# Kernel tuning notes

Hardware: AMD Instinct MI355X
Metric: run time of the kernel (lower is better)

Reference implementation:

```python
import jax, jax.numpy as jnp
import numpy as np

B = 16384      # batch
IN = 151       # input dim (layer_widths[0])
HID = 200      # RBF out_features (layer_widths[1])
CENT = 2000    # layer_centres[0]


def setup_inputs() -> dict:
    key = jax.random.key(0)
    ks = jax.random.split(key, 6)
    x = jax.random.normal(ks[0], (B, IN), dtype=jnp.float32)
    # RBF params per reset_parameters: centres ~ N(0, 0.01), sigmas = 2
    centres = 0.01 * jax.random.normal(ks[1], (HID, IN), dtype=jnp.float32)
    sigmas = jnp.full((HID,), 2.0, dtype=jnp.float32)
    # Linear layers (torch layout: weight is (out, in))
    w1 = jax.random.normal(ks[2], (CENT, HID), dtype=jnp.float32) / jnp.sqrt(jnp.float32(HID))
    b1 = jnp.zeros((CENT,), dtype=jnp.float32)
    # small scale so exp() stays well-conditioned
    w2 = 0.001 * jax.random.normal(ks[3], (CENT, CENT), dtype=jnp.float32)
    b2 = jnp.zeros((CENT,), dtype=jnp.float32)
    # kernel matrix (151, 2000); positive so Ehat[:, 0] > 0
    kern = jax.random.uniform(ks[4], (IN, CENT), dtype=jnp.float32)
    return {"x": x, "centres": centres, "sigmas": sigmas,
            "w1": w1, "b1": b1, "w2": w2, "b2": b2, "kern": kern}


def reference(x, centres, sigmas, w1, b1, w2, b2, kern):
    # RBF layer: distances_ij = ||x_i - c_j||_2 * sigma_j ; phi = exp(-distances^2)
    # exp(-(sqrt(d2)*sigma)^2) == exp(-d2 * sigma^2), so we skip the sqrt and the
    # (B, CENT, IN) expand tensor entirely.
    x2 = jnp.sum(x * x, axis=1, keepdims=True)            # (B, 1)
    c2 = jnp.sum(centres * centres, axis=1)[None, :]      # (1, HID)
    d2 = jnp.maximum(x2 + c2 - 2.0 * (x @ centres.T), 0.0)  # (B, HID)
    phi = jnp.exp(-d2 * (sigmas * sigmas)[None, :])       # (B, HID)

    h = jax.nn.relu(phi @ w1.T + b1)                      # (B, CENT)
    out = jnp.exp(h @ w2.T + b2)                          # (B, CENT)

    Ehat = out @ kern.T                                   # (B, IN)  == matmul(kern, out.T).T
    Rhat = out / Ehat[:, :1]                              # divide by correction term Ehat[:, 0]
    Ehat2 = Rhat @ kern.T                                 # (B, IN)
    return (Ehat2, Rhat, Ehat2, Rhat, x)
```

## Files before the change

### kernel.cpp

```cpp
#include <hip/hip_runtime.h>

#define BDIM 16384
#define IN_D 151
#define HID_D 200
#define CENT_D 2000

#define INP 192
#define HIDP 256
#define CENTP 2048
#define KERNR 256

using bf16x8 = __attribute__((ext_vector_type(8))) short;
using f32x4  = __attribute__((ext_vector_type(4))) float;
using f4     = __attribute__((ext_vector_type(4))) float;
using us4    = __attribute__((ext_vector_type(4))) unsigned short;
using us8    = __attribute__((ext_vector_type(8))) unsigned short;
using i32x4  = __attribute__((ext_vector_type(4))) int;
using i32x8  = __attribute__((ext_vector_type(8))) int;

__device__ __forceinline__ unsigned short f2bf(float f) {
  unsigned u = __builtin_bit_cast(unsigned, f);
  u += 0x7FFFu + ((u >> 16) & 1u);
  return (unsigned short)(u >> 16);
}
__device__ __forceinline__ float bf2f(unsigned short h) {
  unsigned u = ((unsigned)h) << 16;
  return __builtin_bit_cast(float, u);
}
__device__ __forceinline__ unsigned char f2fp8(float f) {
  return (unsigned char)(__builtin_amdgcn_cvt_pk_fp8_f32(f, f, 0, false) & 0xFF);
}

typedef __attribute__((address_space(1))) const unsigned int guint;
typedef __attribute__((address_space(3))) unsigned int luint;
__device__ __forceinline__ void g2l16(const void* g, void* l) {
  __builtin_amdgcn_global_load_lds((guint*)g, (luint*)l, 16, 0, 0);
}

struct GArgs {
  const unsigned short* A;
  const unsigned short* B;
  int K;
  int kspan;
  const float* x2; const float* c2; const float* sg2;
  const float* bias;
  unsigned short* obf; int ldo;
  unsigned char* o8;
  float* of;
};

template<int MODE>
__global__ __launch_bounds__(256) void gemm_bt(GArgs p) {
  __shared__ __align__(16) short As[128 * 64];
  __shared__ __align__(16) short Bs[128 * 64];
  const int tid  = threadIdx.x;
  const int lane = tid & 63;
  const int w    = tid >> 6;
  const int wr   = w >> 1, wc = w & 1;
  const int lr   = lane & 15;
  const int tm = blockIdx.x, tn = blockIdx.y;
  const int K = p.K;
  const int kbeg = blockIdx.z * p.kspan;
  f32x4 acc[4][4] = {};

  const unsigned short* Ag = p.A + (size_t)tm * 128 * K;
  const unsigned short* Bg = p.B + (size_t)tn * 128 * K;

  int rowc[4], colc[4], ldsc[4];
#pragma unroll
  for (int i = 0; i < 4; i++) {
    int cc = i * 256 + tid;
    rowc[i] = cc >> 3;
    colc[i] = ((cc & 7) ^ (rowc[i] & 7)) * 8;
    ldsc[i] = cc * 8;
  }

  for (int k0 = kbeg; k0 < kbeg + p.kspan; k0 += 64) {
    __syncthreads();
#pragma unroll
    for (int i = 0; i < 4; i++)
      g2l16(Ag + (size_t)rowc[i] * K + k0 + colc[i], &As[ldsc[i]]);
#pragma unroll
    for (int i = 0; i < 4; i++)
      g2l16(Bg + (size_t)rowc[i] * K + k0 + colc[i], &Bs[ldsc[i]]);
    __syncthreads();
#pragma unroll
    for (int ks = 0; ks < 2; ks++) {
      bf16x8 af[4], bfr[4];
#pragma unroll
      for (int m = 0; m < 4; m++) {
        int r = wr * 64 + m * 16 + lr;
        af[m] = *(const bf16x8*)&As[r * 64 + ((((ks << 2) + (lane >> 4)) ^ (r & 7)) << 3)];
      }
#pragma unroll
      for (int n = 0; n < 4; n++) {
        int r = wc * 64 + n * 16 + lr;
        bfr[n] = *(const bf16x8*)&Bs[r * 64 + ((((ks << 2) + (lane >> 4)) ^ (r & 7)) << 3)];
      }
#pragma unroll
      for (int m = 0; m < 4; m++)
#pragma unroll
        for (int n = 0; n < 4; n++)
          acc[m][n] = __builtin_amdgcn_mfma_f32_16x16x32_bf16(af[m], bfr[n], acc[m][n], 0, 0, 0);
    }
  }

  const int rb = tm * 128 + wr * 64 + (lane >> 4) * 4;
  const int cb = tn * 128 + wc * 64 + lr;
#pragma unroll
  for (int m = 0; m < 4; m++) {
#pragma unroll
    for (int n = 0; n < 4; n++) {
#pragma unroll
      for (int r = 0; r < 4; r++) {
        const int gi = rb + m * 16 + r;
        const int gj = cb + n * 16;
        const float v = acc[m][n][r];
        if constexpr (MODE == 0) {
          float ph = 0.f;
          if (gj < HID_D) {
            float d2 = fmaxf(p.x2[gi] + p.c2[gj] - 2.f * v, 0.f);
            ph = __expf(-d2 * p.sg2[gj]);
          }
          p.obf[(size_t)gi * p.ldo + gj] = f2bf(ph);
        } else if constexpr (MODE == 1) {
          float b = (gj < CENT_D) ? p.bias[gj] : 0.f;
          p.o8[(size_t)gi * p.ldo + gj] = f2fp8(fmaxf(v + b, 0.f));
        } else {
          float* of = p.of + (size_t)blockIdx.z * BDIM * IN_D;
          if (gj < IN_D) of[(size_t)gi * IN_D + gj] = v;
        }
      }
    }
  }
}

struct G8Args {
  const unsigned char* A;
  const unsigned char* B;
  int K;
  const float* bias;
  unsigned short* obf; int ldo;
};

__global__ __launch_bounds__(256) void gemm_fp8(G8Args p) {
  __shared__ __align__(16) unsigned char As[128 * 128];
  __shared__ __align__(16) unsigned char Bs[128 * 128];
  const int tid  = threadIdx.x;
  const int lane = tid & 63;
  const int w    = tid >> 6;
  const int wr   = w >> 1, wc = w & 1;
  const int lr   = lane & 15;
  const int g    = lane >> 4;
  const int tm = blockIdx.x, tn = blockIdx.y;
  const int K = p.K;
  f32x4 acc[4][4] = {};

  const unsigned char* Ag = p.A + (size_t)tm * 128 * K;
  const unsigned char* Bg = p.B + (size_t)tn * 128 * K;

  int rowc[4], colb[4], ldsb[4];
#pragma unroll
  for (int i = 0; i < 4; i++) {
    int cc = i * 256 + tid;
    rowc[i] = cc >> 3;
    colb[i] = ((cc & 7) ^ (rowc[i] & 7)) << 4;
    ldsb[i] = cc << 4;
  }

  for (int k0 = 0; k0 < K; k0 += 128) {
    __syncthreads();
#pragma unroll
    for (int i = 0; i < 4; i++)
      g2l16(Ag + (size_t)rowc[i] * K + k0 + colb[i], &As[ldsb[i]]);
#pragma unroll
    for (int i = 0; i < 4; i++)
      g2l16(Bg + (size_t)rowc[i] * K + k0 + colb[i], &Bs[ldsb[i]]);
    __syncthreads();

    i32x8 bfr[4];
#pragma unroll
    for (int n = 0; n < 4; n++) {
      const int r = wc * 64 + n * 16 + lr;
      const int rb_ = r << 7, rx = r & 7;
      i32x4 lo = *(const i32x4*)&Bs[rb_ + (((2 * g) ^ rx) << 4)];
      i32x4 hi = *(const i32x4*)&Bs[rb_ + (((2 * g + 1) ^ rx) << 4)];
      bfr[n][0] = lo[0]; bfr[n][1] = lo[1]; bfr[n][2] = lo[2]; bfr[n][3] = lo[3];
      bfr[n][4] = hi[0]; bfr[n][5] = hi[1]; bfr[n][6] = hi[2]; bfr[n][7] = hi[3];
    }
#pragma unroll
    for (int m = 0; m < 4; m++) {
      const int r = wr * 64 + m * 16 + lr;
      const int rb_ = r << 7, rx = r & 7;
      i32x4 lo = *(const i32x4*)&As[rb_ + (((2 * g) ^ rx) << 4)];
      i32x4 hi = *(const i32x4*)&As[rb_ + (((2 * g + 1) ^ rx) << 4)];
      i32x8 av;
      av[0] = lo[0]; av[1] = lo[1]; av[2] = lo[2]; av[3] = lo[3];
      av[4] = hi[0]; av[5] = hi[1]; av[6] = hi[2]; av[7] = hi[3];
#pragma unroll
      for (int n = 0; n < 4; n++)
        acc[m][n] = __builtin_amdgcn_mfma_scale_f32_16x16x128_f8f6f4(
            av, bfr[n], acc[m][n], 0, 0, 0, 127, 0, 127);
    }
  }

  const int rb = tm * 128 + wr * 64 + (lane >> 4) * 4;
  const int cb = tn * 128 + wc * 64 + lr;
  const float rs = 1.0f / 256.0f;
#pragma unroll
  for (int m = 0; m < 4; m++) {
#pragma unroll
    for (int n = 0; n < 4; n++) {
      const int gj = cb + n * 16;
#pragma unroll
      for (int r = 0; r < 4; r++) {
        const int gi = rb + m * 16 + r;
        float o = (gj < CENT_D) ? __expf(acc[m][n][r] * rs + p.bias[gj]) : 0.f;
        p.obf[(size_t)gi * p.ldo + gj] = f2bf(o);
      }
    }
  }
}

__global__ __launch_bounds__(256) void prep_cast(
    const float* __restrict__ x, const float* __restrict__ cen,
    const float* __restrict__ w1, const float* __restrict__ kern,
    unsigned short* __restrict__ x_bf, unsigned short* __restrict__ c_bf,
    unsigned short* __restrict__ w1p, unsigned short* __restrict__ kernp) {
  const int c = blockIdx.x * 256 + threadIdx.x;
  const float* src; unsigned short* dst; int R, C, cpq, local, vec;
  if (c < 786432)       { src = x;    dst = x_bf;  R = 16384; C = 151;  cpq = 48;  local = c;           vec = 0; }
  else if (c < 798720)  { src = cen;  dst = c_bf;  R = 200;   C = 151;  cpq = 48;  local = c - 786432;  vec = 0; }
  else if (c < 929792)  { src = w1;   dst = w1p;   R = 2000;  C = 200;  cpq = 64;  local = c - 798720;  vec = 1; }
  else                  { src = kern; dst = kernp; R = 151;   C = 2000; cpq = 512; local = c - 929792;  vec = 1; }
  const int r  = local / cpq;
  const int c4 = (local - r * cpq) << 2;
  us4 o;
  if (vec && r < R && c4 + 3 < C) {
    f4 v = *(const f4*)&src[(size_t)r * C + c4];
    o[0] = f2bf(v[0]); o[1] = f2bf(v[1]); o[2] = f2bf(v[2]); o[3] = f2bf(v[3]);
  } else {
#pragma unroll
    for (int k = 0; k < 4; k++) {
      float v = (r < R && c4 + k < C) ? src[(size_t)r * C + c4 + k] : 0.f;
      o[k] = f2bf(v);
    }
  }
  *(us4*)&dst[(size_t)local * 4] = o;
}

__global__ __launch_bounds__(256) void cast_fp8(
    const float* __restrict__ src, unsigned char* __restrict__ dst) {
  const int i = blockIdx.x * 256 + threadIdx.x;
  const int r = i >> 9;
  const int c4 = (i & 511) << 2;
  float v0 = 0.f, v1 = 0.f, v2 = 0.f, v3 = 0.f;
  if (r < 2000 && c4 + 3 < 2000) {
    f4 v = *(const f4*)&src[(size_t)r * 2000 + c4];
    v0 = v[0] * 256.f; v1 = v[1] * 256.f; v2 = v[2] * 256.f; v3 = v[3] * 256.f;
  } else if (r < 2000) {
    if (c4 + 0 < 2000) v0 = src[(size_t)r * 2000 + c4 + 0] * 256.f;
    if (c4 + 1 < 2000) v1 = src[(size_t)r * 2000 + c4 + 1] * 256.f;
    if (c4 + 2 < 2000) v2 = src[(size_t)r * 2000 + c4 + 2] * 256.f;
    if (c4 + 3 < 2000) v3 = src[(size_t)r * 2000 + c4 + 3] * 256.f;
  }
  int p0 = __builtin_amdgcn_cvt_pk_fp8_f32(v0, v1, 0, false);
  int p1 = __builtin_amdgcn_cvt_pk_fp8_f32(v2, v3, 0, false);
  unsigned int packed = ((unsigned)p0 & 0xFFFFu) | (((unsigned)p1 & 0xFFFFu) << 16);
  *(unsigned int*)&dst[(size_t)i * 4] = packed;
}

__global__ __launch_bounds__(256) void prep_misc(
    const float* __restrict__ x, const float* __restrict__ cen,
    const float* __restrict__ sg,
    float* __restrict__ x2, float* __restrict__ c2, float* __restrict__ sg2) {
  const int b = blockIdx.x;
  if (b == 4160) {
    int j = threadIdx.x;
    sg2[j] = (j < HID_D) ? sg[j] * sg[j] : 0.f;
    return;
  }
  const float* src; float* dst; int R, base;
  if (b < 4096) { src = x;   dst = x2; R = BDIM;  base = b * 4; }
  else          { src = cen; dst = c2; R = HID_D; base = (b - 4096) * 4; }
  const int row = base + (threadIdx.x >> 6);
  const int l = threadIdx.x & 63;
  float s = 0.f;
  if (row < R)
    for (int k = l; k < IN_D; k += 64) { float v = src[(size_t)row * IN_D + k]; s += v * v; }
#pragma unroll
  for (int off = 32; off > 0; off >>= 1) s += __shfl_down(s, off);
  if (l == 0) dst[row] = s;
}

__global__ __launch_bounds__(256) void finalize(
    float* __restrict__ dout, const unsigned short* __restrict__ outp,
    const float* __restrict__ x, const float* __restrict__ part) {
  const int i = blockIdx.x;
  const size_t SL = (size_t)BDIM * IN_D;
  float* Eh = dout;
  float* Ra = dout + SL;
  float* Eb = dout + SL + (size_t)BDIM * CENT_D;
  float* Rb = Eb + SL;
  float* xo = Rb + (size_t)BDIM * CENT_D;
  const size_t ib = (size_t)i * IN_D;
  const float e0 = part[ib] + part[SL + ib] + part[2 * SL + ib] + part[3 * SL + ib];
  const float s = 1.f / e0;
  const int t = threadIdx.x;
  if (t < IN_D) {
    float v = (part[ib + t] + part[SL + ib + t] + part[2 * SL + ib + t] + part[3 * SL + ib + t]) * s;
    Eh[ib + t] = v;
    Eb[ib + t] = v;
    xo[ib + t] = x[ib + t];
  }
  if (t < 250) {
    const us8 u = *(const us8*)&outp[(size_t)i * CENTP + t * 8];
    f4 a, b;
#pragma unroll
    for (int k = 0; k < 4; k++) a[k] = bf2f(u[k]) * s;
#pragma unroll
    for (int k = 0; k < 4; k++) b[k] = bf2f(u[4 + k]) * s;
    const size_t o = (size_t)i * CENT_D + t * 8;
    *(f4*)&Ra[o] = a; *(f4*)&Ra[o + 4] = b;
    *(f4*)&Rb[o] = a; *(f4*)&Rb[o + 4] = b;
  }
}

extern "C" void kernel_launch(void* const* d_in, const int* in_sizes, int n_in,
                              void* d_out, int out_size, void* d_ws, size_t ws_size,
                              hipStream_t stream) {
  (void)in_sizes; (void)n_in; (void)out_size; (void)ws_size;
  const float* x       = (const float*)d_in[0];
  const float* centres = (const float*)d_in[1];
  const float* sigmas  = (const float*)d_in[2];
  const float* w1      = (const float*)d_in[3];
  const float* b1      = (const float*)d_in[4];
  const float* w2      = (const float*)d_in[5];
  const float* b2      = (const float*)d_in[6];
  const float* kern    = (const float*)d_in[7];
  float* dout = (float*)d_out;

  char* ws = (char*)d_ws;
  size_t off = 0;
  auto alloc = [&](size_t bytes) {
    char* p = ws + off;
    off = (off + bytes + 255) & ~(size_t)255;
    return p;
  };
  unsigned short* x_bf  = (unsigned short*)alloc((size_t)BDIM * INP * 2);
  unsigned short* c_bf  = (unsigned short*)alloc((size_t)KERNR * INP * 2);
  unsigned short* w1p   = (unsigned short*)alloc((size_t)CENTP * HIDP * 2);
  unsigned char*  w2p8  = (unsigned char*)alloc((size_t)CENTP * CENTP);
  unsigned short* kernp = (unsigned short*)alloc((size_t)KERNR * CENTP * 2);
  unsigned short* phip  = (unsigned short*)alloc((size_t)BDIM * HIDP * 2);
  unsigned short* outp  = (unsigned short*)alloc((size_t)BDIM * CENTP * 2);
  float* x2  = (float*)alloc((size_t)BDIM * 4);
  float* c2  = (float*)alloc((size_t)KERNR * 4);
  float* sg2 = (float*)alloc((size_t)KERNR * 4);
  float* eparts = (float*)alloc((size_t)4 * BDIM * IN_D * 4);
  unsigned char* hp8 = (unsigned char*)(dout + (size_t)BDIM * (2 * IN_D + CENT_D));

  prep_cast<<<4144, 256, 0, stream>>>(x, centres, w1, kern, x_bf, c_bf, w1p, kernp);
  cast_fp8<<<4096, 256, 0, stream>>>(w2, w2p8);
  prep_misc<<<4161, 256, 0, stream>>>(x, centres, sigmas, x2, c2, sg2);

  GArgs g0{}; g0.A = x_bf; g0.B = c_bf; g0.K = INP; g0.kspan = INP;
  g0.x2 = x2; g0.c2 = c2; g0.sg2 = sg2; g0.obf = phip; g0.ldo = HIDP;
  gemm_bt<0><<<dim3(BDIM / 128, HIDP / 128, 1), 256, 0, stream>>>(g0);

  GArgs g1{}; g1.A = phip; g1.B = w1p; g1.K = HIDP; g1.kspan = HIDP;
  g1.bias = b1; g1.o8 = hp8; g1.ldo = CENTP;
  gemm_bt<1><<<dim3(BDIM / 128, CENTP / 128, 1), 256, 0, stream>>>(g1);

  G8Args g2{}; g2.A = hp8; g2.B = w2p8; g2.K = CENTP;
  g2.bias = b2; g2.obf = outp; g2.ldo = CENTP;
  gemm_fp8<<<dim3(BDIM / 128, CENTP / 128), 256, 0, stream>>>(g2);

  GArgs g3{}; g3.A = outp; g3.B = kernp; g3.K = CENTP; g3.kspan = CENTP / 4;
  g3.of = eparts;
  gemm_bt<3><<<dim3(BDIM / 128, KERNR / 128, 4), 256, 0, stream>>>(g3);

  finalize<<<BDIM, 256, 0, stream>>>(dout, outp, x, eparts);
}
```

Baseline: 280.3 us.

## Quantize hidden activations and second weight matrix to FP4 with FP8 first layer

The RBF output phi and the first-layer weights are now stored as FP8, so the first linear layer runs on the FP8 scaled MFMA. Its ReLU output h is packed to FP4 (two values per byte via a lane shuffle). The large second GEMM then runs as an FP4 x FP4 scaled MFMA against a 512-scaled FP4 copy of w2. This halves operand bytes for the dominant GEMM and uses the higher-rate FP4 matrix path. In exchange it adds heavy quantization error from a coarse 8-level FP4 grid applied to both h and w2, a branchy software FP4 encoder in the epilogue, and zero-padded halves in the MFMA operand registers.

```diff
diff --git a/kernel.cpp b/kernel.cpp
--- a/kernel.cpp
+++ b/kernel.cpp
@@ -30,6 +30,20 @@
 __device__ __forceinline__ unsigned char f2fp8(float f) {
   return (unsigned char)(__builtin_amdgcn_cvt_pk_fp8_f32(f, f, 0, false) & 0xFF);
 }
+__device__ __forceinline__ unsigned f2fp4(float f) {
+  float a = fabsf(f);
+  unsigned s = (__builtin_bit_cast(unsigned, f) >> 31) << 3;
+  unsigned m;
+  if      (a < 0.25f) m = 0;
+  else if (a < 0.75f) m = 1;
+  else if (a < 1.25f) m = 2;
+  else if (a < 1.75f) m = 3;
+  else if (a < 2.5f)  m = 4;
+  else if (a < 3.5f)  m = 5;
+  else if (a < 5.0f)  m = 6;
+  else                m = 7;
+  return s | m;
+}
 
 typedef __attribute__((address_space(1))) const unsigned int guint;
 typedef __attribute__((address_space(3))) unsigned int luint;
@@ -43,9 +57,7 @@
   int K;
   int kspan;
   const float* x2; const float* c2; const float* sg2;
-  const float* bias;
-  unsigned short* obf; int ldo;
-  unsigned char* o8;
+  unsigned char* o8; int ldo;
   float* of;
 };
 
@@ -122,10 +134,7 @@
             float d2 = fmaxf(p.x2[gi] + p.c2[gj] - 2.f * v, 0.f);
             ph = __expf(-d2 * p.sg2[gj]);
           }
-          p.obf[(size_t)gi * p.ldo + gj] = f2bf(ph);
-        } else if constexpr (MODE == 1) {
-          float b = (gj < CENT_D) ? p.bias[gj] : 0.f;
-          p.o8[(size_t)gi * p.ldo + gj] = f2fp8(fmaxf(v + b, 0.f));
+          p.o8[(size_t)gi * p.ldo + gj] = f2fp8(ph);
         } else {
           float* of = p.of + (size_t)blockIdx.z * BDIM * IN_D;
           if (gj < IN_D) of[(size_t)gi * IN_D + gj] = v;
@@ -135,15 +144,14 @@
   }
 }
 
-struct G8Args {
+struct GhArgs {
   const unsigned char* A;
   const unsigned char* B;
-  int K;
   const float* bias;
-  unsigned short* obf; int ldo;
+  unsigned char* o4;
 };
 
-__global__ __launch_bounds__(256) void gemm_fp8(G8Args p) {
+__global__ __launch_bounds__(256) void gemm_h(GhArgs p) {
   __shared__ __align__(16) unsigned char As[128 * 128];
   __shared__ __align__(16) unsigned char Bs[128 * 128];
   const int tid  = threadIdx.x;
@@ -153,11 +161,10 @@
   const int lr   = lane & 15;
   const int g    = lane >> 4;
   const int tm = blockIdx.x, tn = blockIdx.y;
-  const int K = p.K;
   f32x4 acc[4][4] = {};
 
-  const unsigned char* Ag = p.A + (size_t)tm * 128 * K;
-  const unsigned char* Bg = p.B + (size_t)tn * 128 * K;
+  const unsigned char* Ag = p.A + (size_t)tm * 128 * 256;
+  const unsigned char* Bg = p.B + (size_t)tn * 128 * 256;
 
   int rowc[4], colb[4], ldsb[4];
 #pragma unroll
@@ -168,14 +175,15 @@
     ldsb[i] = cc << 4;
   }
 
-  for (int k0 = 0; k0 < K; k0 += 128) {
-    __syncthreads();
-#pragma unroll
-    for (int i = 0; i < 4; i++)
-      g2l16(Ag + (size_t)rowc[i] * K + k0 + colb[i], &As[ldsb[i]]);
-#pragma unroll
-    for (int i = 0; i < 4; i++)
-      g2l16(Bg + (size_t)rowc[i] * K + k0 + colb[i], &Bs[ldsb[i]]);
+#pragma unroll
+  for (int k0 = 0; k0 < 256; k0 += 128) {
+    __syncthreads();
+#pragma unroll
+    for (int i = 0; i < 4; i++)
+      g2l16(Ag + (size_t)rowc[i] * 256 + k0 + colb[i], &As[ldsb[i]]);
+#pragma unroll
+    for (int i = 0; i < 4; i++)
+      g2l16(Bg + (size_t)rowc[i] * 256 + k0 + colb[i], &Bs[ldsb[i]]);
     __syncthreads();
 
     i32x8 bfr[4];
@@ -206,7 +214,98 @@
 
   const int rb = tm * 128 + wr * 64 + (lane >> 4) * 4;
   const int cb = tn * 128 + wc * 64 + lr;
-  const float rs = 1.0f / 256.0f;
+  const float rs = 0.125f;
+#pragma unroll
+  for (int m = 0; m < 4; m++) {
+#pragma unroll
+    for (int n = 0; n < 4; n++) {
+      const int gj = cb + n * 16;
+      const float b = (gj < CENT_D) ? p.bias[gj] : 0.f;
+#pragma unroll
+      for (int r = 0; r < 4; r++) {
+        const int gi = rb + m * 16 + r;
+        float hv = fmaxf(acc[m][n][r] * rs + b, 0.f);
+        float ov = __shfl_xor(hv, 1);
+        if (!(lane & 1))
+          p.o4[(size_t)gi * 1024 + (gj >> 1)] =
+              (unsigned char)(f2fp4(hv) | (f2fp4(ov) << 4));
+      }
+    }
+  }
+}
+
+struct G4Args {
+  const unsigned char* A;
+  const unsigned char* B;
+  const float* bias;
+  unsigned short* obf;
+};
+
+__global__ __launch_bounds__(256) void gemm_fp4(G4Args p) {
+  __shared__ __align__(16) unsigned char As[128 * 128];
+  __shared__ __align__(16) unsigned char Bs[128 * 128];
+  const int tid  = threadIdx.x;
+  const int lane = tid & 63;
+  const int w    = tid >> 6;
+  const int wr   = w >> 1, wc = w & 1;
+  const int lr   = lane & 15;
+  const int g    = lane >> 4;
+  const int tm = blockIdx.x, tn = blockIdx.y;
+  const int KB = CENTP / 2;
+  f32x4 acc[4][4] = {};
+
+  const unsigned char* Ag = p.A + (size_t)tm * 128 * KB;
+  const unsigned char* Bg = p.B + (size_t)tn * 128 * KB;
+
+  int rowc[4], colb[4], ldsb[4];
+#pragma unroll
+  for (int i = 0; i < 4; i++) {
+    int cc = i * 256 + tid;
+    rowc[i] = cc >> 3;
+    colb[i] = ((cc & 7) ^ (rowc[i] & 7)) << 4;
+    ldsb[i] = cc << 4;
+  }
+
+  for (int kb0 = 0; kb0 < KB; kb0 += 128) {
+    __syncthreads();
+#pragma unroll
+    for (int i = 0; i < 4; i++)
+      g2l16(Ag + (size_t)rowc[i] * KB + kb0 + colb[i], &As[ldsb[i]]);
+#pragma unroll
+    for (int i = 0; i < 4; i++)
+      g2l16(Bg + (size_t)rowc[i] * KB + kb0 + colb[i], &Bs[ldsb[i]]);
+    __syncthreads();
+
+#pragma unroll
+    for (int ks = 0; ks < 2; ks++) {
+      i32x8 bfr[4];
+#pragma unroll
+      for (int n = 0; n < 4; n++) {
+        const int r = wc * 64 + n * 16 + lr;
+        const int rb_ = r << 7, rx = r & 7;
+        i32x4 v = *(const i32x4*)&Bs[rb_ + ((((ks << 2) + g) ^ rx) << 4)];
+        bfr[n][0] = v[0]; bfr[n][1] = v[1]; bfr[n][2] = v[2]; bfr[n][3] = v[3];
+        bfr[n][4] = 0; bfr[n][5] = 0; bfr[n][6] = 0; bfr[n][7] = 0;
+      }
+#pragma unroll
+      for (int m = 0; m < 4; m++) {
+        const int r = wr * 64 + m * 16 + lr;
+        const int rb_ = r << 7, rx = r & 7;
+        i32x4 v = *(const i32x4*)&As[rb_ + ((((ks << 2) + g) ^ rx) << 4)];
+        i32x8 av;
+        av[0] = v[0]; av[1] = v[1]; av[2] = v[2]; av[3] = v[3];
+        av[4] = 0; av[5] = 0; av[6] = 0; av[7] = 0;
+#pragma unroll
+        for (int n = 0; n < 4; n++)
+          acc[m][n] = __builtin_amdgcn_mfma_scale_f32_16x16x128_f8f6f4(
+              av, bfr[n], acc[m][n], 4, 4, 0, 127, 0, 127);
+      }
+    }
+  }
+
+  const int rb = tm * 128 + wr * 64 + (lane >> 4) * 4;
+  const int cb = tn * 128 + wc * 64 + lr;
+  const float rs = 1.0f / 512.0f;
 #pragma unroll
   for (int m = 0; m < 4; m++) {
 #pragma unroll
@@ -216,7 +315,7 @@
       for (int r = 0; r < 4; r++) {
         const int gi = rb + m * 16 + r;
         float o = (gj < CENT_D) ? __expf(acc[m][n][r] * rs + p.bias[gj]) : 0.f;
-        p.obf[(size_t)gi * p.ldo + gj] = f2bf(o);
+        p.obf[(size_t)gi * CENTP + gj] = f2bf(o);
       }
     }
   }
@@ -224,15 +323,14 @@
 
 __global__ __launch_bounds__(256) void prep_cast(
     const float* __restrict__ x, const float* __restrict__ cen,
-    const float* __restrict__ w1, const float* __restrict__ kern,
+    const float* __restrict__ kern,
     unsigned short* __restrict__ x_bf, unsigned short* __restrict__ c_bf,
-    unsigned short* __restrict__ w1p, unsigned short* __restrict__ kernp) {
+    unsigned short* __restrict__ kernp) {
   const int c = blockIdx.x * 256 + threadIdx.x;
   const float* src; unsigned short* dst; int R, C, cpq, local, vec;
   if (c < 786432)       { src = x;    dst = x_bf;  R = 16384; C = 151;  cpq = 48;  local = c;           vec = 0; }
   else if (c < 798720)  { src = cen;  dst = c_bf;  R = 200;   C = 151;  cpq = 48;  local = c - 786432;  vec = 0; }
-  else if (c < 929792)  { src = w1;   dst = w1p;   R = 2000;  C = 200;  cpq = 64;  local = c - 798720;  vec = 1; }
-  else                  { src = kern; dst = kernp; R = 151;   C = 2000; cpq = 512; local = c - 929792;  vec = 1; }
+  else                  { src = kern; dst = kernp; R = 151;   C = 2000; cpq = 512; local = c - 798720;  vec = 1; }
   const int r  = local / cpq;
   const int c4 = (local - r * cpq) << 2;
   us4 o;
@@ -249,25 +347,33 @@
   *(us4*)&dst[(size_t)local * 4] = o;
 }
 
-__global__ __launch_bounds__(256) void cast_fp8(
-    const float* __restrict__ src, unsigned char* __restrict__ dst) {
+__global__ __launch_bounds__(256) void prep_lowp(
+    const float* __restrict__ w1, const float* __restrict__ w2,
+    unsigned char* __restrict__ w1p8, unsigned char* __restrict__ w2p4) {
   const int i = blockIdx.x * 256 + threadIdx.x;
-  const int r = i >> 9;
-  const int c4 = (i & 511) << 2;
-  float v0 = 0.f, v1 = 0.f, v2 = 0.f, v3 = 0.f;
-  if (r < 2000 && c4 + 3 < 2000) {
-    f4 v = *(const f4*)&src[(size_t)r * 2000 + c4];
-    v0 = v[0] * 256.f; v1 = v[1] * 256.f; v2 = v[2] * 256.f; v3 = v[3] * 256.f;
-  } else if (r < 2000) {
-    if (c4 + 0 < 2000) v0 = src[(size_t)r * 2000 + c4 + 0] * 256.f;
-    if (c4 + 1 < 2000) v1 = src[(size_t)r * 2000 + c4 + 1] * 256.f;
-    if (c4 + 2 < 2000) v2 = src[(size_t)r * 2000 + c4 + 2] * 256.f;
-    if (c4 + 3 < 2000) v3 = src[(size_t)r * 2000 + c4 + 3] * 256.f;
-  }
-  int p0 = __builtin_amdgcn_cvt_pk_fp8_f32(v0, v1, 0, false);
-  int p1 = __builtin_amdgcn_cvt_pk_fp8_f32(v2, v3, 0, false);
-  unsigned int packed = ((unsigned)p0 & 0xFFFFu) | (((unsigned)p1 & 0xFFFFu) << 16);
-  *(unsigned int*)&dst[(size_t)i * 4] = packed;
+  if (i < 131072) {
+    const int r = i >> 6;
+    const int c4 = (i & 63) << 2;
+    float v[4];
+#pragma unroll
+    for (int k = 0; k < 4; k++)
+      v[k] = (r < 2000 && c4 + k < 200) ? w1[(size_t)r * 200 + c4 + k] * 8.f : 0.f;
+    int p0 = __builtin_amdgcn_cvt_pk_fp8_f32(v[0], v[1], 0, false);
+    int p1 = __builtin_amdgcn_cvt_pk_fp8_f32(v[2], v[3], 0, false);
+    *(unsigned int*)&w1p8[(size_t)i * 4] =
+        ((unsigned)p0 & 0xFFFFu) | (((unsigned)p1 & 0xFFFFu) << 16);
+  } else {
+    const int j = i - 131072;
+    const int r = j >> 8;
+    const int c8 = (j & 255) << 3;
+    unsigned u = 0;
+#pragma unroll
+    for (int k = 0; k < 8; k++) {
+      float v = (r < 2000 && c8 + k < 2000) ? w2[(size_t)r * 2000 + c8 + k] * 512.f : 0.f;
+      u |= f2fp4(v) << (4 * k);
+    }
+    *(unsigned int*)&w2p4[(size_t)j * 4] = u;
+  }
 }
 
 __global__ __launch_bounds__(256) void prep_misc(
@@ -349,32 +455,30 @@
   };
   unsigned short* x_bf  = (unsigned short*)alloc((size_t)BDIM * INP * 2);
   unsigned short* c_bf  = (unsigned short*)alloc((size_t)KERNR * INP * 2);
-  unsigned short* w1p   = (unsigned short*)alloc((size_t)CENTP * HIDP * 2);
-  unsigned char*  w2p8  = (unsigned char*)alloc((size_t)CENTP * CENTP);
+  unsigned char*  w1p8  = (unsigned char*)alloc((size_t)CENTP * HIDP);
+  unsigned char*  w2p4  = (unsigned char*)alloc((size_t)CENTP * CENTP / 2);
   unsigned short* kernp = (unsigned short*)alloc((size_t)KERNR * CENTP * 2);
-  unsigned short* phip  = (unsigned short*)alloc((size_t)BDIM * HIDP * 2);
+  unsigned char*  phip8 = (unsigned char*)alloc((size_t)BDIM * HIDP);
   unsigned short* outp  = (unsigned short*)alloc((size_t)BDIM * CENTP * 2);
   float* x2  = (float*)alloc((size_t)BDIM * 4);
   float* c2  = (float*)alloc((size_t)KERNR * 4);
   float* sg2 = (float*)alloc((size_t)KERNR * 4);
   float* eparts = (float*)alloc((size_t)4 * BDIM * IN_D * 4);
-  unsigned char* hp8 = (unsigned char*)(dout + (size_t)BDIM * (2 * IN_D + CENT_D));
-
-  prep_cast<<<4144, 256, 0, stream>>>(x, centres, w1, kern, x_bf, c_bf, w1p, kernp);
-  cast_fp8<<<4096, 256, 0, stream>>>(w2, w2p8);
+  unsigned char* hp4 = (unsigned char*)(dout + (size_t)BDIM * (2 * IN_D + CENT_D));
+
+  prep_cast<<<3632, 256, 0, stream>>>(x, centres, kern, x_bf, c_bf, kernp);
+  prep_lowp<<<2560, 256, 0, stream>>>(w1, w2, w1p8, w2p4);
   prep_misc<<<4161, 256, 0, stream>>>(x, centres, sigmas, x2, c2, sg2);
 
   GArgs g0{}; g0.A = x_bf; g0.B = c_bf; g0.K = INP; g0.kspan = INP;
-  g0.x2 = x2; g0.c2 = c2; g0.sg2 = sg2; g0.obf = phip; g0.ldo = HIDP;
+  g0.x2 = x2; g0.c2 = c2; g0.sg2 = sg2; g0.o8 = phip8; g0.ldo = HIDP;
   gemm_bt<0><<<dim3(BDIM / 128, HIDP / 128, 1), 256, 0, stream>>>(g0);
 
-  GArgs g1{}; g1.A = phip; g1.B = w1p; g1.K = HIDP; g1.kspan = HIDP;
-  g1.bias = b1; g1.o8 = hp8; g1.ldo = CENTP;
-  gemm_bt<1><<<dim3(BDIM / 128, CENTP / 128, 1), 256, 0, stream>>>(g1);
-
-  G8Args g2{}; g2.A = hp8; g2.B = w2p8; g2.K = CENTP;
-  g2.bias = b2; g2.obf = outp; g2.ldo = CENTP;
-  gemm_fp8<<<dim3(BDIM / 128, CENTP / 128), 256, 0, stream>>>(g2);
+  GhArgs g1{}; g1.A = phip8; g1.B = w1p8; g1.bias = b1; g1.o4 = hp4;
+  gemm_h<<<dim3(BDIM / 128, CENTP / 128), 256, 0, stream>>>(g1);
+
+  G4Args g2{}; g2.A = hp4; g2.B = w2p4; g2.bias = b2; g2.obf = outp;
+  gemm_fp4<<<dim3(BDIM / 128, CENTP / 128), 256, 0, stream>>>(g2);
 
   GArgs g3{}; g3.A = outp; g3.B = kernp; g3.K = CENTP; g3.kspan = CENTP / 4;
   g3.of = eparts;
```

Result: slower. 361.5 us (+29.0%).

## Switch hidden-layer GEMM from FP8 to FP4 MFMA with repacked operands

Applied to the files above, without the earlier changes.

Quantizes both the relu activations and w2 to FP4 (E2M1) and runs the 2000x2000 GEMM with the f8f6f4 scaled MFMA in fp4 mode, halving operand bytes and doubling K per tile load. The activations are still produced as FP8 by the previous GEMM and then repacked to FP4 by an extra pass, so a full read and write of the activation matrix is added. Quantizing to 8-level FP4 with fixed scales risks large accuracy loss for the exp() output, and the MFMA calls zero-fill the upper operand registers.

```diff
diff --git a/kernel.cpp b/kernel.cpp
--- a/kernel.cpp
+++ b/kernel.cpp
@@ -29,6 +29,27 @@
 }
 __device__ __forceinline__ unsigned char f2fp8(float f) {
   return (unsigned char)(__builtin_amdgcn_cvt_pk_fp8_f32(f, f, 0, false) & 0xFF);
+}
+__device__ __forceinline__ float fp8d(unsigned b) {
+  unsigned s = b >> 7, e = (b >> 3) & 15, m = b & 7;
+  unsigned fb = (s << 31) | ((e + 120) << 23) | (m << 20);
+  float nrm = __builtin_bit_cast(float, fb);
+  float sub = (s ? -1.f : 1.f) * (float)m * 0.001953125f;
+  return e ? nrm : sub;
+}
+__device__ __forceinline__ unsigned f2fp4(float f) {
+  float a = fabsf(f);
+  unsigned s = (__builtin_bit_cast(unsigned, f) >> 31) << 3;
+  unsigned m;
+  if      (a < 0.25f) m = 0;
+  else if (a < 0.75f) m = 1;
+  else if (a < 1.25f) m = 2;
+  else if (a < 1.75f) m = 3;
+  else if (a < 2.5f)  m = 4;
+  else if (a < 3.5f)  m = 5;
+  else if (a < 5.0f)  m = 6;
+  else                m = 7;
+  return s | m;
 }
 
 typedef __attribute__((address_space(1))) const unsigned int guint;
@@ -135,15 +156,14 @@
   }
 }
 
-struct G8Args {
+struct G4Args {
   const unsigned char* A;
   const unsigned char* B;
-  int K;
   const float* bias;
-  unsigned short* obf; int ldo;
+  unsigned short* obf;
 };
 
-__global__ __launch_bounds__(256) void gemm_fp8(G8Args p) {
+__global__ __launch_bounds__(256) void gemm_fp4(G4Args p) {
   __shared__ __align__(16) unsigned char As[128 * 128];
   __shared__ __align__(16) unsigned char Bs[128 * 128];
   const int tid  = threadIdx.x;
@@ -153,11 +173,11 @@
   const int lr   = lane & 15;
   const int g    = lane >> 4;
   const int tm = blockIdx.x, tn = blockIdx.y;
-  const int K = p.K;
+  const int KB = CENTP / 2;
   f32x4 acc[4][4] = {};
 
-  const unsigned char* Ag = p.A + (size_t)tm * 128 * K;
-  const unsigned char* Bg = p.B + (size_t)tn * 128 * K;
+  const unsigned char* Ag = p.A + (size_t)tm * 128 * KB;
+  const unsigned char* Bg = p.B + (size_t)tn * 128 * KB;
 
   int rowc[4], colb[4], ldsb[4];
 #pragma unroll
@@ -168,45 +188,46 @@
     ldsb[i] = cc << 4;
   }
 
-  for (int k0 = 0; k0 < K; k0 += 128) {
+  for (int kb0 = 0; kb0 < KB; kb0 += 128) {
     __syncthreads();
 #pragma unroll
     for (int i = 0; i < 4; i++)
-      g2l16(Ag + (size_t)rowc[i] * K + k0 + colb[i], &As[ldsb[i]]);
+      g2l16(Ag + (size_t)rowc[i] * KB + kb0 + colb[i], &As[ldsb[i]]);
 #pragma unroll
     for (int i = 0; i < 4; i++)
-      g2l16(Bg + (size_t)rowc[i] * K + k0 + colb[i], &Bs[ldsb[i]]);
+      g2l16(Bg + (size_t)rowc[i] * KB + kb0 + colb[i], &Bs[ldsb[i]]);
     __syncthreads();
 
-    i32x8 bfr[4];
-#pragma unroll
-    for (int n = 0; n < 4; n++) {
-      const int r = wc * 64 + n * 16 + lr;
-      const int rb_ = r << 7, rx = r & 7;
-      i32x4 lo = *(const i32x4*)&Bs[rb_ + (((2 * g) ^ rx) << 4)];
-      i32x4 hi = *(const i32x4*)&Bs[rb_ + (((2 * g + 1) ^ rx) << 4)];
-      bfr[n][0] = lo[0]; bfr[n][1] = lo[1]; bfr[n][2] = lo[2]; bfr[n][3] = lo[3];
-      bfr[n][4] = hi[0]; bfr[n][5] = hi[1]; bfr[n][6] = hi[2]; bfr[n][7] = hi[3];
-    }
-#pragma unroll
-    for (int m = 0; m < 4; m++) {
-      const int r = wr * 64 + m * 16 + lr;
-      const int rb_ = r << 7, rx = r & 7;
-      i32x4 lo = *(const i32x4*)&As[rb_ + (((2 * g) ^ rx) << 4)];
-      i32x4 hi = *(const i32x4*)&As[rb_ + (((2 * g + 1) ^ rx) << 4)];
-      i32x8 av;
-      av[0] = lo[0]; av[1] = lo[1]; av[2] = lo[2]; av[3] = lo[3];
-      av[4] = hi[0]; av[5] = hi[1]; av[6] = hi[2]; av[7] = hi[3];
-#pragma unroll
-      for (int n = 0; n < 4; n++)
-        acc[m][n] = __builtin_amdgcn_mfma_scale_f32_16x16x128_f8f6f4(
-            av, bfr[n], acc[m][n], 0, 0, 0, 127, 0, 127);
+#pragma unroll
+    for (int ks = 0; ks < 2; ks++) {
+      i32x8 bfr[4];
+#pragma unroll
+      for (int n = 0; n < 4; n++) {
+        const int r = wc * 64 + n * 16 + lr;
+        const int rb_ = r << 7, rx = r & 7;
+        i32x4 v = *(const i32x4*)&Bs[rb_ + ((((ks << 2) + g) ^ rx) << 4)];
+        bfr[n][0] = v[0]; bfr[n][1] = v[1]; bfr[n][2] = v[2]; bfr[n][3] = v[3];
+        bfr[n][4] = 0; bfr[n][5] = 0; bfr[n][6] = 0; bfr[n][7] = 0;
+      }
+#pragma unroll
+      for (int m = 0; m < 4; m++) {
+        const int r = wr * 64 + m * 16 + lr;
+        const int rb_ = r << 7, rx = r & 7;
+        i32x4 v = *(const i32x4*)&As[rb_ + ((((ks << 2) + g) ^ rx) << 4)];
+        i32x8 av;
+        av[0] = v[0]; av[1] = v[1]; av[2] = v[2]; av[3] = v[3];
+        av[4] = 0; av[5] = 0; av[6] = 0; av[7] = 0;
+#pragma unroll
+        for (int n = 0; n < 4; n++)
+          acc[m][n] = __builtin_amdgcn_mfma_scale_f32_16x16x128_f8f6f4(
+              av, bfr[n], acc[m][n], 4, 4, 0, 127, 0, 127);
+      }
     }
   }
 
   const int rb = tm * 128 + wr * 64 + (lane >> 4) * 4;
   const int cb = tn * 128 + wc * 64 + lr;
-  const float rs = 1.0f / 256.0f;
+  const float rs = 1.0f / 512.0f;
 #pragma unroll
   for (int m = 0; m < 4; m++) {
 #pragma unroll
@@ -216,10 +237,21 @@
       for (int r = 0; r < 4; r++) {
         const int gi = rb + m * 16 + r;
         float o = (gj < CENT_D) ? __expf(acc[m][n][r] * rs + p.bias[gj]) : 0.f;
-        p.obf[(size_t)gi * p.ldo + gj] = f2bf(o);
+        p.obf[(size_t)gi * CENTP + gj] = f2bf(o);
       }
     }
   }
+}
+
+__global__ __launch_bounds__(256) void repack8to4(
+    const unsigned long long* __restrict__ src, unsigned int* __restrict__ dst) {
+  const size_t i = (size_t)blockIdx.x * 256 + threadIdx.x;
+  unsigned long long v = src[i];
+  unsigned u = 0;
+#pragma unroll
+  for (int k = 0; k < 8; k++)
+    u |= f2fp4(fp8d((unsigned)(v >> (8 * k)) & 0xFFu)) << (4 * k);
+  dst[i] = u;
 }
 
 __global__ __launch_bounds__(256) void prep_cast(
@@ -249,25 +281,18 @@
   *(us4*)&dst[(size_t)local * 4] = o;
 }
 
-__global__ __launch_bounds__(256) void cast_fp8(
-    const float* __restrict__ src, unsigned char* __restrict__ dst) {
-  const int i = blockIdx.x * 256 + threadIdx.x;
-  const int r = i >> 9;
-  const int c4 = (i & 511) << 2;
-  float v0 = 0.f, v1 = 0.f, v2 = 0.f, v3 = 0.f;
-  if (r < 2000 && c4 + 3 < 2000) {
-    f4 v = *(const f4*)&src[(size_t)r * 2000 + c4];
-    v0 = v[0] * 256.f; v1 = v[1] * 256.f; v2 = v[2] * 256.f; v3 = v[3] * 256.f;
-  } else if (r < 2000) {
-    if (c4 + 0 < 2000) v0 = src[(size_t)r * 2000 + c4 + 0] * 256.f;
-    if (c4 + 1 < 2000) v1 = src[(size_t)r * 2000 + c4 + 1] * 256.f;
-    if (c4 + 2 < 2000) v2 = src[(size_t)r * 2000 + c4 + 2] * 256.f;
-    if (c4 + 3 < 2000) v3 = src[(size_t)r * 2000 + c4 + 3] * 256.f;
-  }
-  int p0 = __builtin_amdgcn_cvt_pk_fp8_f32(v0, v1, 0, false);
-  int p1 = __builtin_amdgcn_cvt_pk_fp8_f32(v2, v3, 0, false);
-  unsigned int packed = ((unsigned)p0 & 0xFFFFu) | (((unsigned)p1 & 0xFFFFu) << 16);
-  *(unsigned int*)&dst[(size_t)i * 4] = packed;
+__global__ __launch_bounds__(256) void cast_fp4(
+    const float* __restrict__ src, unsigned int* __restrict__ dst) {
+  const int j = blockIdx.x * 256 + threadIdx.x;
+  const int r = j >> 8;
+  const int c8 = (j & 255) << 3;
+  unsigned u = 0;
+#pragma unroll
+  for (int k = 0; k < 8; k++) {
+    float v = (r < 2000 && c8 + k < 2000) ? src[(size_t)r * 2000 + c8 + k] * 512.f : 0.f;
+    u |= f2fp4(v) << (4 * k);
+  }
+  dst[j] = u;
 }
 
 __global__ __launch_bounds__(256) void prep_misc(
@@ -350,10 +375,11 @@
   unsigned short* x_bf  = (unsigned short*)alloc((size_t)BDIM * INP * 2);
   unsigned short* c_bf  = (unsigned short*)alloc((size_t)KERNR * INP * 2);
   unsigned short* w1p   = (unsigned short*)alloc((size_t)CENTP * HIDP * 2);
-  unsigned char*  w2p8  = (unsigned char*)alloc((size_t)CENTP * CENTP);
+  unsigned int*   w2p4  = (unsigned int*)alloc((size_t)CENTP * CENTP / 2);
   unsigned short* kernp = (unsigned short*)alloc((size_t)KERNR * CENTP * 2);
   unsigned short* phip  = (unsigned short*)alloc((size_t)BDIM * HIDP * 2);
   unsigned short* outp  = (unsigned short*)alloc((size_t)BDIM * CENTP * 2);
+  unsigned int*   hp4   = (unsigned int*)alloc((size_t)BDIM * CENTP / 2);
   float* x2  = (float*)alloc((size_t)BDIM * 4);
   float* c2  = (float*)alloc((size_t)KERNR * 4);
   float* sg2 = (float*)alloc((size_t)KERNR * 4);
@@ -361,7 +387,7 @@
   unsigned char* hp8 = (unsigned char*)(dout + (size_t)BDIM * (2 * IN_D + CENT_D));
 
   prep_cast<<<4144, 256, 0, stream>>>(x, centres, w1, kern, x_bf, c_bf, w1p, kernp);
-  cast_fp8<<<4096, 256, 0, stream>>>(w2, w2p8);
+  cast_fp4<<<2048, 256, 0, stream>>>(w2, w2p4);
   prep_misc<<<4161, 256, 0, stream>>>(x, centres, sigmas, x2, c2, sg2);
 
   GArgs g0{}; g0.A = x_bf; g0.B = c_bf; g0.K = INP; g0.kspan = INP;
@@ -372,9 +398,12 @@
   g1.bias = b1; g1.o8 = hp8; g1.ldo = CENTP;
   gemm_bt<1><<<dim3(BDIM / 128, CENTP / 128, 1), 256, 0, stream>>>(g1);
 
-  G8Args g2{}; g2.A = hp8; g2.B = w2p8; g2.K = CENTP;
-  g2.bias = b2; g2.obf = outp; g2.ldo = CENTP;
-  gemm_fp8<<<dim3(BDIM / 128, CENTP / 128), 256, 0, stream>>>(g2);
+  repack8to4<<<(int)((size_t)BDIM * CENTP / 8 / 256), 256, 0, stream>>>(
+      (const unsigned long long*)hp8, hp4);
+
+  G4Args g2{}; g2.A = (const unsigned char*)hp4; g2.B = (const unsigned char*)w2p4;
+  g2.bias = b2; g2.obf = outp;
+  gemm_fp4<<<dim3(BDIM / 128, CENTP / 128), 256, 0, stream>>>(g2);
 
   GArgs g3{}; g3.A = outp; g3.B = kernp; g3.K = CENTP; g3.kspan = CENTP / 4;
   g3.of = eparts;
```

After: 375.9 us. 1.34x slower.

## Use FP8 for first linear layer and widen final GEMM tile to 192 columns

Applied to the files above, without the earlier changes.

Stores RBF activations and w1 as FP8 (w1 prescaled by 8) and runs the first linear layer through the FP8 MFMA GEMM with a relu epilogue. The kern GEMM gets a dedicated kernel with a 128x192 tile, so kern is padded to 192 rows instead of 256 and redundant A-tile loads and MFMAs are removed. This cuts bytes moved and padded compute, at the cost of lower precision in the first layer.

```diff
diff --git a/kernel.cpp b/kernel.cpp
--- a/kernel.cpp
+++ b/kernel.cpp
@@ -8,7 +8,7 @@
 #define INP 192
 #define HIDP 256
 #define CENTP 2048
-#define KERNR 256
+#define KERN_R 192
 
 using bf16x8 = __attribute__((ext_vector_type(8))) short;
 using f32x4  = __attribute__((ext_vector_type(4))) float;
@@ -37,20 +37,14 @@
   __builtin_amdgcn_global_load_lds((guint*)g, (luint*)l, 16, 0, 0);
 }
 
-struct GArgs {
+struct G0Args {
   const unsigned short* A;
   const unsigned short* B;
-  int K;
-  int kspan;
   const float* x2; const float* c2; const float* sg2;
-  const float* bias;
-  unsigned short* obf; int ldo;
   unsigned char* o8;
-  float* of;
 };
 
-template<int MODE>
-__global__ __launch_bounds__(256) void gemm_bt(GArgs p) {
+__global__ __launch_bounds__(256) void gemm_phi(G0Args p) {
   __shared__ __align__(16) short As[128 * 64];
   __shared__ __align__(16) short Bs[128 * 64];
   const int tid  = threadIdx.x;
@@ -59,12 +53,10 @@
   const int wr   = w >> 1, wc = w & 1;
   const int lr   = lane & 15;
   const int tm = blockIdx.x, tn = blockIdx.y;
-  const int K = p.K;
-  const int kbeg = blockIdx.z * p.kspan;
   f32x4 acc[4][4] = {};
 
-  const unsigned short* Ag = p.A + (size_t)tm * 128 * K;
-  const unsigned short* Bg = p.B + (size_t)tn * 128 * K;
+  const unsigned short* Ag = p.A + (size_t)tm * 128 * INP;
+  const unsigned short* Bg = p.B + (size_t)tn * 128 * INP;
 
   int rowc[4], colc[4], ldsc[4];
 #pragma unroll
@@ -75,14 +67,14 @@
     ldsc[i] = cc * 8;
   }
 
-  for (int k0 = kbeg; k0 < kbeg + p.kspan; k0 += 64) {
+  for (int k0 = 0; k0 < INP; k0 += 64) {
     __syncthreads();
 #pragma unroll
     for (int i = 0; i < 4; i++)
-      g2l16(Ag + (size_t)rowc[i] * K + k0 + colc[i], &As[ldsc[i]]);
+      g2l16(Ag + (size_t)rowc[i] * INP + k0 + colc[i], &As[ldsc[i]]);
 #pragma unroll
     for (int i = 0; i < 4; i++)
-      g2l16(Bg + (size_t)rowc[i] * K + k0 + colc[i], &Bs[ldsc[i]]);
+      g2l16(Bg + (size_t)rowc[i] * INP + k0 + colc[i], &Bs[ldsc[i]]);
     __syncthreads();
 #pragma unroll
     for (int ks = 0; ks < 2; ks++) {
@@ -111,25 +103,16 @@
   for (int m = 0; m < 4; m++) {
 #pragma unroll
     for (int n = 0; n < 4; n++) {
+      const int gj = cb + n * 16;
 #pragma unroll
       for (int r = 0; r < 4; r++) {
         const int gi = rb + m * 16 + r;
-        const int gj = cb + n * 16;
-        const float v = acc[m][n][r];
-        if constexpr (MODE == 0) {
-          float ph = 0.f;
-          if (gj < HID_D) {
-            float d2 = fmaxf(p.x2[gi] + p.c2[gj] - 2.f * v, 0.f);
-            ph = __expf(-d2 * p.sg2[gj]);
-          }
-          p.obf[(size_t)gi * p.ldo + gj] = f2bf(ph);
-        } else if constexpr (MODE == 1) {
-          float b = (gj < CENT_D) ? p.bias[gj] : 0.f;
-          p.o8[(size_t)gi * p.ldo + gj] = f2fp8(fmaxf(v + b, 0.f));
-        } else {
-          float* of = p.of + (size_t)blockIdx.z * BDIM * IN_D;
-          if (gj < IN_D) of[(size_t)gi * IN_D + gj] = v;
+        float ph = 0.f;
+        if (gj < HID_D) {
+          float d2 = fmaxf(p.x2[gi] + p.c2[gj] - 2.f * acc[m][n][r], 0.f);
+          ph = __expf(-d2 * p.sg2[gj]);
         }
+        p.o8[(size_t)gi * HIDP + gj] = f2fp8(ph);
       }
     }
   }
@@ -140,9 +123,11 @@
   const unsigned char* B;
   int K;
   const float* bias;
-  unsigned short* obf; int ldo;
+  unsigned short* obf;
+  unsigned char* o8;
 };
 
+template<int MODE>
 __global__ __launch_bounds__(256) void gemm_fp8(G8Args p) {
   __shared__ __align__(16) unsigned char As[128 * 128];
   __shared__ __align__(16) unsigned char Bs[128 * 128];
@@ -206,17 +191,108 @@
 
   const int rb = tm * 128 + wr * 64 + (lane >> 4) * 4;
   const int cb = tn * 128 + wc * 64 + lr;
-  const float rs = 1.0f / 256.0f;
+  const float rs = (MODE == 1) ? 0.125f : (1.0f / 256.0f);
 #pragma unroll
   for (int m = 0; m < 4; m++) {
 #pragma unroll
     for (int n = 0; n < 4; n++) {
       const int gj = cb + n * 16;
+      const float b = (gj < CENT_D) ? p.bias[gj] : 0.f;
 #pragma unroll
       for (int r = 0; r < 4; r++) {
         const int gi = rb + m * 16 + r;
-        float o = (gj < CENT_D) ? __expf(acc[m][n][r] * rs + p.bias[gj]) : 0.f;
-        p.obf[(size_t)gi * p.ldo + gj] = f2bf(o);
+        if constexpr (MODE == 1) {
+          p.o8[(size_t)gi * CENTP + gj] = f2fp8(fmaxf(acc[m][n][r] * rs + b, 0.f));
+        } else {
+          float o = (gj < CENT_D) ? __expf(acc[m][n][r] * rs + b) : 0.f;
+          p.obf[(size_t)gi * CENTP + gj] = f2bf(o);
+        }
+      }
+    }
+  }
+}
+
+struct G3Args {
+  const unsigned short* A;
+  const unsigned short* B;
+  float* of;
+  int kspan;
+};
+
+__global__ __launch_bounds__(256, 1) void gemm3w(G3Args p) {
+  __shared__ __align__(16) short As[128 * 64];
+  __shared__ __align__(16) short Bs[KERN_R * 64];
+  const int tid  = threadIdx.x;
+  const int lane = tid & 63;
+  const int w    = tid >> 6;
+  const int wr   = w >> 1, wc = w & 1;
+  const int lr   = lane & 15;
+  const int tm = blockIdx.x;
+  const int kbeg = blockIdx.y * p.kspan;
+  f32x4 acc[4][6] = {};
+
+  const unsigned short* Ag = p.A + (size_t)tm * 128 * CENTP;
+  const unsigned short* Bg = p.B;
+
+  int rowa[4], cola[4], lda_[4];
+#pragma unroll
+  for (int i = 0; i < 4; i++) {
+    int cc = i * 256 + tid;
+    rowa[i] = cc >> 3;
+    cola[i] = ((cc & 7) ^ (rowa[i] & 7)) * 8;
+    lda_[i] = cc * 8;
+  }
+  int rowb[6], colbb[6], ldb_[6];
+#pragma unroll
+  for (int i = 0; i < 6; i++) {
+    int cc = i * 256 + tid;
+    rowb[i] = cc >> 3;
+    colbb[i] = ((cc & 7) ^ (rowb[i] & 7)) * 8;
+    ldb_[i] = cc * 8;
+  }
+
+  for (int k0 = kbeg; k0 < kbeg + p.kspan; k0 += 64) {
+    __syncthreads();
+#pragma unroll
+    for (int i = 0; i < 4; i++)
+      g2l16(Ag + (size_t)rowa[i] * CENTP + k0 + cola[i], &As[lda_[i]]);
+#pragma unroll
+    for (int i = 0; i < 6; i++)
+      g2l16(Bg + (size_t)rowb[i] * CENTP + k0 + colbb[i], &Bs[ldb_[i]]);
+    __syncthreads();
+#pragma unroll
+    for (int ks = 0; ks < 2; ks++) {
+      bf16x8 af[4], bfr[6];
+#pragma unroll
+      for (int m = 0; m < 4; m++) {
+        int r = wr * 64 + m * 16 + lr;
+        af[m] = *(const bf16x8*)&As[r * 64 + ((((ks << 2) + (lane >> 4)) ^ (r & 7)) << 3)];
+      }
+#pragma unroll
+      for (int n = 0; n < 6; n++) {
+        int r = wc * 96 + n * 16 + lr;
+        bfr[n] = *(const bf16x8*)&Bs[r * 64 + ((((ks << 2) + (lane >> 4)) ^ (r & 7)) << 3)];
+      }
+#pragma unroll
+      for (int m = 0; m < 4; m++)
+#pragma unroll
+        for (int n = 0; n < 6; n++)
+          acc[m][n] = __builtin_amdgcn_mfma_f32_16x16x32_bf16(af[m], bfr[n], acc[m][n], 0, 0, 0);
+    }
+  }
+
+  float* of = p.of + (size_t)blockIdx.y * BDIM * IN_D;
+  const int rb = tm * 128 + wr * 64 + (lane >> 4) * 4;
+  const int cb = wc * 96 + lr;
+#pragma unroll
+  for (int m = 0; m < 4; m++) {
+#pragma unroll
+    for (int n = 0; n < 6; n++) {
+      const int gj = cb + n * 16;
+#pragma unroll
+      for (int r = 0; r < 4; r++) {
+        const int gi = rb + m * 16 + r;
+        if (gj < IN_D) of[(size_t)gi * IN_D + gj] = acc[m][n][r];
       }
     }
   }
@@ -224,15 +300,14 @@
 
 __global__ __launch_bounds__(256) void prep_cast(
     const float* __restrict__ x, const float* __restrict__ cen,
-    const float* __restrict__ w1, const float* __restrict__ kern,
+    const float* __restrict__ kern,
     unsigned short* __restrict__ x_bf, unsigned short* __restrict__ c_bf,
-    unsigned short* __restrict__ w1p, unsigned short* __restrict__ kernp) {
+    unsigned short* __restrict__ kernp) {
   const int c = blockIdx.x * 256 + threadIdx.x;
   const float* src; unsigned short* dst; int R, C, cpq, local, vec;
   if (c < 786432)       { src = x;    dst = x_bf;  R = 16384; C = 151;  cpq = 48;  local = c;           vec = 0; }
   else if (c < 798720)  { src = cen;  dst = c_bf;  R = 200;   C = 151;  cpq = 48;  local = c - 786432;  vec = 0; }
-  else if (c < 929792)  { src = w1;   dst = w1p;   R = 2000;  C = 200;  cpq = 64;  local = c - 798720;  vec = 1; }
-  else                  { src = kern; dst = kernp; R = 151;   C = 2000; cpq = 512; local = c - 929792;  vec = 1; }
+  else                  { src = kern; dst = kernp; R = 151;   C = 2000; cpq = 512; local = c - 798720;  vec = 1; }
   const int r  = local / cpq;
   const int c4 = (local - r * cpq) << 2;
   us4 o;
@@ -249,25 +324,22 @@
   *(us4*)&dst[(size_t)local * 4] = o;
 }
 
-__global__ __launch_bounds__(256) void cast_fp8(
-    const float* __restrict__ src, unsigned char* __restrict__ dst) {
+__global__ __launch_bounds__(256) void prep_lowp(
+    const float* __restrict__ w1, const float* __restrict__ w2,
+    unsigned char* __restrict__ w1p8, unsigned char* __restrict__ w2p8) {
   const int i = blockIdx.x * 256 + threadIdx.x;
-  const int r = i >> 9;
-  const int c4 = (i & 511) << 2;
-  float v0 = 0.f, v1 = 0.f, v2 = 0.f, v3 = 0.f;
-  if (r < 2000 && c4 + 3 < 2000) {
-    f4 v = *(const f4*)&src[(size_t)r * 2000 + c4];
-    v0 = v[0] * 256.f; v1 = v[1] * 256.f; v2 = v[2] * 256.f; v3 = v[3] * 256.f;
-  } else if (r < 2000) {
-    if (c4 + 0 < 2000) v0 = src[(size_t)r * 2000 + c4 + 0] * 256.f;
-    if (c4 + 1 < 2000) v1 = src[(size_t)r * 2000 + c4 + 1] * 256.f;
-    if (c4 + 2 < 2000) v2 = src[(size_t)r * 2000 + c4 + 2] * 256.f;
-    if (c4 + 3 < 2000) v3 = src[(size_t)r * 2000 + c4 + 3] * 256.f;
-  }
-  int p0 = __builtin_amdgcn_cvt_pk_fp8_f32(v0, v1, 0, false);
-  int p1 = __builtin_amdgcn_cvt_pk_fp8_f32(v2, v3, 0, false);
-  unsigned int packed = ((unsigned)p0 & 0xFFFFu) | (((unsigned)p1 & 0xFFFFu) << 16);
-  *(unsigned int*)&dst[(size_t)i * 4] = packed;
+  const float* src; unsigned char* dst; int r, c4, R, C; float sc;
+  int j;
+  if (i < 131072) { src = w1; dst = w1p8; j = i;          r = j >> 6; c4 = (j & 63) << 2;  R = 2000; C = 200;  sc = 8.f; }
+  else            { src = w2; dst = w2p8; j = i - 131072; r = j >> 9; c4 = (j & 511) << 2; R = 2000; C = 2000; sc = 256.f; }
+  float v[4];
+#pragma unroll
+  for (int k = 0; k < 4; k++)
+    v[k] = (r < R && c4 + k < C) ? src[(size_t)r * C + c4 + k] * sc : 0.f;
+  int p0 = __builtin_amdgcn_cvt_pk_fp8_f32(v[0], v[1], 0, false);
+  int p1 = __builtin_amdgcn_cvt_pk_fp8_f32(v[2], v[3], 0, false);
+  *(unsigned int*)&dst[(size_t)j * 4] =
+      ((unsigned)p0 & 0xFFFFu) | (((unsigned)p1 & 0xFFFFu) << 16);
 }
 
 __global__ __launch_bounds__(256) void prep_misc(
@@ -348,37 +420,36 @@
     return p;
   };
   unsigned short* x_bf  = (unsigned short*)alloc((size_t)BDIM * INP * 2);
-  unsigned short* c_bf  = (unsigned short*)alloc((size_t)KERNR * INP * 2);
-  unsigned short* w1p   = (unsigned short*)alloc((size_t)CENTP * HIDP * 2);
+  unsigned short* c_bf  = (unsigned short*)alloc((size_t)256 * INP * 2);
+  unsigned char*  w1p8  = (unsigned char*)alloc((size_t)CENTP * HIDP);
   unsigned char*  w2p8  = (unsigned char*)alloc((size_t)CENTP * CENTP);
-  unsigned short* kernp = (unsigned short*)alloc((size_t)KERNR * CENTP * 2);
-  unsigned short* phip  = (unsigned short*)alloc((size_t)BDIM * HIDP * 2);
+  unsigned short* kernp = (unsigned short*)alloc((size_t)KERN_R * CENTP * 2);
+  unsigned char*  phip8 = (unsigned char*)alloc((size_t)BDIM * HIDP);
   unsigned short* outp  = (unsigned short*)alloc((size_t)BDIM * CENTP * 2);
   float* x2  = (float*)alloc((size_t)BDIM * 4);
-  float* c2  = (float*)alloc((size_t)KERNR * 4);
-  float* sg2 = (float*)alloc((size_t)KERNR * 4);
+  float* c2  = (float*)alloc((size_t)256 * 4);
+  float* sg2 = (float*)alloc((size_t)256 * 4);
   float* eparts = (float*)alloc((size_t)4 * BDIM * IN_D * 4);
   unsigned char* hp8 = (unsigned char*)(dout + (size_t)BDIM * (2 * IN_D + CENT_D));
 
-  prep_cast<<<4144, 256, 0, stream>>>(x, centres, w1, kern, x_bf, c_bf, w1p, kernp);
-  cast_fp8<<<4096, 256, 0, stream>>>(w2, w2p8);
+  prep_cast<<<3504, 256, 0, stream>>>(x, centres, kern, x_bf, c_bf, kernp);
+  prep_lowp<<<4608, 256, 0, stream>>>(w1, w2, w1p8, w2p8);
   prep_misc<<<4161, 256, 0, stream>>>(x, centres, sigmas, x2, c2, sg2);
 
-  GArgs g0{}; g0.A = x_bf; g0.B = c_bf; g0.K = INP; g0.kspan = INP;
-  g0.x2 = x2; g0.c2 = c2; g0.sg2 = sg2; g0.obf = phip; g0.ldo = HIDP;
-  gemm_bt<0><<<dim3(BDIM / 128, HIDP / 128, 1), 256, 0, stream>>>(g0);
-
-  GArgs g1{}; g1.A = phip; g1.B = w1p; g1.K = HIDP; g1.kspan = HIDP;
-  g1.bias = b1; g1.o8 = hp8; g1.ldo = CENTP;
-  gemm_bt<1><<<dim3(BDIM / 128, CENTP / 128, 1), 256, 0, stream>>>(g1);
+  G0Args g0{}; g0.A = x_bf; g0.B = c_bf;
+  g0.x2 = x2; g0.c2 = c2; g0.sg2 = sg2; g0.o8 = phip8;
+  gemm_phi<<<dim3(BDIM / 128, HIDP / 128), 256, 0, stream>>>(g0);
+
+  G8Args g1{}; g1.A = phip8; g1.B = w1p8; g1.K = HIDP;
+  g1.bias = b1; g1.o8 = hp8;
+  gemm_fp8<1><<<dim3(BDIM / 128, CENTP / 128), 256, 0, stream>>>(g1);
 
   G8Args g2{}; g2.A = hp8; g2.B = w2p8; g2.K = CENTP;
-  g2.bias = b2; g2.obf = outp; g2.ldo = CENTP;
-  gemm_fp8<<<dim3(BDIM / 128, CENTP / 128), 256, 0, stream>>>(g2);
-
-  GArgs g3{}; g3.A = outp; g3.B = kernp; g3.K = CENTP; g3.kspan = CENTP / 4;
-  g3.of = eparts;
-  gemm_bt<3><<<dim3(BDIM / 128, KERNR / 128, 4), 256, 0, stream>>>(g3);
+  g2.bias = b2; g2.obf = outp;
+  gemm_fp8<2><<<dim3(BDIM / 128, CENTP / 128), 256, 0, stream>>>(g2);
+
+  G3Args g3{}; g3.A = outp; g3.B = kernp; g3.of = eparts; g3.kspan = CENTP / 4;
+  gemm3w<<<dim3(BDIM / 128, 4), 256, 0, stream>>>(g3);
 
   finalize<<<BDIM, 256, 0, stream>>>(dout, outp, x, eparts);
 }
```

Result: faster. 244.3 us (-12.8%).
